# Optimization experiments

Hardware: AMD Instinct MI355X
Metric: run time of the kernel (lower is better)

The kernel has to match this reference:

```python
import jax, jax.numpy as jnp
import numpy as np

N, E, NF, EF, G = 50000, 400000, 128, 64, 200


def _leaky(x):
    return jax.nn.leaky_relu(x, 0.01)


def _edge_softmax(logits, dst, n):
    # softmax over edges grouped by destination node; logits: [E, 1]
    m = jax.ops.segment_max(logits, dst, num_segments=n)
    m = jnp.where(jnp.isfinite(m), m, 0.0)  # guard empty segments
    e = jnp.exp(logits - m[dst])
    s = jax.ops.segment_sum(e, dst, num_segments=n)
    return e / s[dst]


def _gru(x, h, Wx, Wh, bx, bh):
    # torch.nn.GRUCell gate order: (r, z, n)
    gx = x @ Wx + bx
    gh = h @ Wh + bh
    H = h.shape[-1]
    r = jax.nn.sigmoid(gx[:, :H] + gh[:, :H])
    z = jax.nn.sigmoid(gx[:, H:2 * H] + gh[:, H:2 * H])
    nn_ = jnp.tanh(gx[:, 2 * H:] + r * gh[:, 2 * H:])
    return (1.0 - z) * nn_ + z * h


def setup_inputs() -> dict:
    key = jax.random.key(0)
    ks = jax.random.split(key, 20)
    f32 = jnp.float32
    w = lambda k, s: (jax.random.normal(k, s) * 0.05).astype(f32)
    z = lambda s: jnp.zeros(s, f32)
    return {
        "node_feats": jax.random.normal(ks[0], (N, NF), f32),
        "edge_feats": jax.random.normal(ks[1], (E, EF), f32),
        "gc_node_W": w(ks[4], (NF, G)), "gc_node_b": z((G,)),
        "gc_e1_W": w(ks[5], (NF + EF, G)), "gc_e1_b": z((G,)),
        "gc_e2_W": w(ks[6], (2 * G, 1)), "gc_e2_b": z((1,)),
        "gc_et_W": w(ks[7], (G, G)), "gc_et_b": z((G,)),
        "gc_gru_Wx": w(ks[8], (G, 3 * G)), "gc_gru_Wh": w(ks[9], (G, 3 * G)),
        "gc_gru_bx": z((3 * G,)), "gc_gru_bh": z((3 * G,)),
        "l1_e_W": w(ks[10], (2 * G, 1)), "l1_e_b": z((1,)),
        "l1_pn_W": w(ks[11], (G, G)), "l1_pn_b": z((G,)),
        "l1_gru_Wx": w(ks[12], (G, 3 * G)), "l1_gru_Wh": w(ks[13], (G, 3 * G)),
        "l1_gru_bx": z((3 * G,)), "l1_gru_bh": z((3 * G,)),
        "l1_bn_g": jnp.ones((G,), f32), "l1_bn_b": z((G,)),
        "src": jax.random.randint(ks[2], (E,), 0, N, jnp.int32),
        "dst": jax.random.randint(ks[3], (E,), 0, N, jnp.int32),
    }


def reference(node_feats, edge_feats,
              gc_node_W, gc_node_b, gc_e1_W, gc_e1_b, gc_e2_W, gc_e2_b,
              gc_et_W, gc_et_b, gc_gru_Wx, gc_gru_Wh, gc_gru_bx, gc_gru_bh,
              l1_e_W, l1_e_b, l1_pn_W, l1_pn_b, l1_gru_Wx, l1_gru_Wh,
              l1_gru_bx, l1_gru_bh, l1_bn_g, l1_bn_b, src, dst):
    n = node_feats.shape[0]
    # ---- GetContext ----
    hv_new = _leaky(node_feats @ gc_node_W + gc_node_b)                      # [N, G]
    he1 = _leaky(jnp.concatenate([node_feats[src], edge_feats], 1)
                 @ gc_e1_W + gc_e1_b)                                        # [E, G]
    logits = _leaky(jnp.concatenate([hv_new[dst], he1], 1)
                    @ gc_e2_W + gc_e2_b)                                     # [E, 1]
    a = _edge_softmax(logits, dst, n)
    e = a * (he1 @ gc_et_W + gc_et_b)
    c = jax.ops.segment_sum(e, dst, num_segments=n)                          # [N, G]
    h0 = jax.nn.relu(_gru(jax.nn.elu(c), hv_new,
                          gc_gru_Wx, gc_gru_Wh, gc_gru_bx, gc_gru_bh))
    # ---- GNNLayer ----
    logits2 = _leaky(jnp.concatenate([h0[dst], h0[src]], 1) @ l1_e_W + l1_e_b)
    a2 = _edge_softmax(logits2, dst, n) + 1.0
    hvp = h0 @ l1_pn_W + l1_pn_b
    c2 = jax.ops.segment_sum(hvp[src] * a2, dst, num_segments=n)
    h1 = jax.nn.relu(_gru(jax.nn.elu(c2), h0,
                          l1_gru_Wx, l1_gru_Wh, l1_gru_bx, l1_gru_bh))
    # BatchNorm1d (training-mode batch stats, eps=1e-5)
    mu = h1.mean(0)
    var = h1.var(0)
    h1 = l1_bn_g * (h1 - mu) / jnp.sqrt(var + 1e-5) + l1_bn_b
    return h0 + h1
```

## Files before the change

kernel.cpp:

```cpp
#include <hip/hip_runtime.h>
#include <math.h>

#define G 200
#define NF 128
#define EF 64

typedef __attribute__((ext_vector_type(8))) short bf16x8;
typedef __attribute__((ext_vector_type(4))) float f32x4;

__device__ __forceinline__ float leakyf(float x) { return x > 0.f ? x : 0.01f * x; }
__device__ __forceinline__ float eluf(float x)   { return x > 0.f ? x : (expf(x) - 1.f); }
__device__ __forceinline__ float sigm(float x)   { return 1.f / (1.f + expf(-x)); }

__device__ __forceinline__ unsigned short f2bf(float x) {
    union { float f; unsigned int u; } v; v.f = x;
    unsigned int r = v.u + 0x7FFF + ((v.u >> 16) & 1);
    return (unsigned short)(r >> 16);
}
__device__ __forceinline__ float bf2f(unsigned short u) {
    union { unsigned int i; float f; } v; v.i = ((unsigned int)u) << 16;
    return v.f;
}
__device__ __forceinline__ unsigned int pk2(float a, float b) {
    return (unsigned int)f2bf(a) | ((unsigned int)f2bf(b) << 16);
}

__global__ __launch_bounds__(256) void tprep_k(
    const float* __restrict__ W, unsigned short* __restrict__ Wt,
    int Kreal, int kpad, int Nstride, int Nreal)
{
    int total = 208 * kpad;
    for (int i = blockIdx.x * 256 + threadIdx.x; i < total; i += gridDim.x * 256) {
        int n = i / kpad, k = i % kpad;
        Wt[i] = (n < Nreal && k < Kreal) ? f2bf(W[(size_t)k * Nstride + n]) : 0;
    }
}

__global__ __launch_bounds__(256) void wgru3_k(
    const float* __restrict__ Wx, const float* __restrict__ Wh,
    unsigned short* __restrict__ Btrz, unsigned short* __restrict__ Btn)
{
    const int total = 512 * 416;
    for (int i = blockIdx.x * 256 + threadIdx.x; i < total; i += gridDim.x * 256) {
        int n = i / 416, k = i % 416;
        float v = 0.f;
        if (n < 416) {
            int gg = (n >= 208) ? 1 : 0;
            int c = n - gg * 208;
            if (c < 200) {
                if (k < 200)                  v = Wx[(size_t)k * 600 + gg * 200 + c];
                else if (k >= 208 && k < 408) v = Wh[(size_t)(k - 208) * 600 + gg * 200 + c];
            }
        }
        Btrz[i] = f2bf(v);

        float u = 0.f;
        int s = n >> 4, cc = n & 15;
        if (s < 26) {
            int c = (s >> 1) * 16 + cc;
            if (c < 200) {
                if (!(s & 1)) { if (k < 200) u = Wx[(size_t)k * 600 + 400 + c]; }
                else { if (k >= 208 && k < 408) u = Wh[(size_t)(k - 208) * 600 + 400 + c]; }
            }
        }
        Btn[i] = f2bf(u);
    }
}

__global__ __launch_bounds__(256) void gpack_k(
    const float* __restrict__ X, const float* __restrict__ H,
    unsigned short* __restrict__ Apk, int M, int Mpad)
{
    const long total = (long)Mpad * 52;
    for (long i = (long)blockIdx.x * 256 + threadIdx.x; i < total;
         i += (long)gridDim.x * 256) {
        int row = (int)(i / 52), ch = (int)(i % 52);
        uint4 u = make_uint4(0, 0, 0, 0);
        if (row < M) {
            if (ch < 25) {
                const float4* xp = (const float4*)(X + (size_t)row * 200 + ch * 8);
                float4 a = xp[0], b = xp[1];
                u.x = pk2(eluf(a.x), eluf(a.y)); u.y = pk2(eluf(a.z), eluf(a.w));
                u.z = pk2(eluf(b.x), eluf(b.y)); u.w = pk2(eluf(b.z), eluf(b.w));
            } else if (ch >= 26 && ch < 51) {
                const float4* hp = (const float4*)(H + (size_t)row * 200 + (ch - 26) * 8);
                float4 a = hp[0], b = hp[1];
                u.x = pk2(a.x, a.y); u.y = pk2(a.z, a.w);
                u.z = pk2(b.x, b.y); u.w = pk2(b.z, b.w);
            }
        }
        *(uint4*)&Apk[(size_t)row * 416 + ch * 8] = u;
    }
}

template <int EPI>
__global__ __launch_bounds__(256) void tgemm_k(
    const unsigned short* __restrict__ Apk,
    const unsigned short* __restrict__ Bt,
    const float* __restrict__ bx, const float* __restrict__ bh,
    unsigned short* __restrict__ RZ,
    float* __restrict__ OUT, int M)
{
    __shared__ __align__(16) unsigned short As[2][128 * 32];
    __shared__ __align__(16) unsigned short Bs[2][128 * 32];

    const int tid = threadIdx.x;
    const int w = tid >> 6, lane = tid & 63, l15 = lane & 15, lq = lane >> 4;
    const int wr = w >> 1, wc = w & 1;
    const int bm = blockIdx.x * 128, bn = blockIdx.y * 128;
    const int r0 = tid >> 2, sl = tid & 3;

    f32x4 acc[4][4];
#pragma unroll
    for (int a = 0; a < 4; ++a)
#pragma unroll
        for (int b = 0; b < 4; ++b) acc[a][b] = (f32x4){0.f, 0.f, 0.f, 0.f};

    {
        uint4 pa0 = *(const uint4*)&Apk[(size_t)(bm + r0) * 416 + sl * 8];
        uint4 pa1 = *(const uint4*)&Apk[(size_t)(bm + 64 + r0) * 416 + sl * 8];
        uint4 pb0 = *(const uint4*)&Bt[(size_t)(bn + r0) * 416 + sl * 8];
        uint4 pb1 = *(const uint4*)&Bt[(size_t)(bn + 64 + r0) * 416 + sl * 8];
        int w0 = sl ^ ((r0 >> 1) & 3), w1 = sl ^ (((r0 + 64) >> 1) & 3);
        *(uint4*)&As[0][r0 * 32 + w0 * 8] = pa0;
        *(uint4*)&As[0][(r0 + 64) * 32 + w1 * 8] = pa1;
        *(uint4*)&Bs[0][r0 * 32 + w0 * 8] = pb0;
        *(uint4*)&Bs[0][(r0 + 64) * 32 + w1 * 8] = pb1;
    }
    __syncthreads();

    int cur = 0;
    for (int c = 0; c < 13; ++c) {
        uint4 pa0, pa1, pb0, pb1;
        if (c < 12) {
            int kc = (c + 1) * 32;
            pa0 = *(const uint4*)&Apk[(size_t)(bm + r0) * 416 + kc + sl * 8];
            pa1 = *(const uint4*)&Apk[(size_t)(bm + 64 + r0) * 416 + kc + sl * 8];
            pb0 = *(const uint4*)&Bt[(size_t)(bn + r0) * 416 + kc + sl * 8];
            pb1 = *(const uint4*)&Bt[(size_t)(bn + 64 + r0) * 416 + kc + sl * 8];
        }
        bf16x8 af[4], bfr[4];
#pragma unroll
        for (int s = 0; s < 4; ++s) {
            int ra = wr * 64 + s * 16 + l15;
            af[s] = *(const bf16x8*)&As[cur][ra * 32 + (lq ^ ((ra >> 1) & 3)) * 8];
            int rb = wc * 64 + s * 16 + l15;
            bfr[s] = *(const bf16x8*)&Bs[cur][rb * 32 + (lq ^ ((rb >> 1) & 3)) * 8];
        }
#pragma unroll
        for (int sr = 0; sr < 4; ++sr)
#pragma unroll
            for (int sc = 0; sc < 4; ++sc)
                acc[sr][sc] = __builtin_amdgcn_mfma_f32_16x16x32_bf16(
                    af[sr], bfr[sc], acc[sr][sc], 0, 0, 0);

        if (c < 12) {
            int nb = cur ^ 1;
            int w0 = sl ^ ((r0 >> 1) & 3), w1 = sl ^ (((r0 + 64) >> 1) & 3);
            *(uint4*)&As[nb][r0 * 32 + w0 * 8] = pa0;
            *(uint4*)&As[nb][(r0 + 64) * 32 + w1 * 8] = pa1;
            *(uint4*)&Bs[nb][r0 * 32 + w0 * 8] = pb0;
            *(uint4*)&Bs[nb][(r0 + 64) * 32 + w1 * 8] = pb1;
        }
        __syncthreads();
        cur ^= 1;
    }

    if (EPI == 0) {
#pragma unroll
        for (int sr = 0; sr < 4; ++sr)
#pragma unroll
            for (int sc = 0; sc < 4; ++sc) {
                int col = bn + wc * 64 + sc * 16 + l15;
                if (col >= 416) continue;
                float bsum = (col < 208) ? (bx[col] + bh[col])
                                         : (bx[col - 8] + bh[col - 8]);
#pragma unroll
                for (int i = 0; i < 4; ++i) {
                    int row = bm + wr * 64 + sr * 16 + lq * 4 + i;
                    if (row < M)
                        RZ[(size_t)row * 416 + col] = f2bf(sigm(acc[sr][sc][i] + bsum));
                }
            }
    } else {
#pragma unroll
        for (int p = 0; p < 2; ++p) {
            int sglob = (bn >> 4) + wc * 4 + 2 * p;
            int cc = (sglob >> 1) * 16 + l15;
            if (cc >= 200) continue;
            float bxn = bx[400 + cc], bhn = bh[400 + cc];
#pragma unroll
            for (int sr = 0; sr < 4; ++sr)
#pragma unroll
                for (int i = 0; i < 4; ++i) {
                    int row = bm + wr * 64 + sr * 16 + lq * 4 + i;
                    if (row >= M) continue;
                    float rr = bf2f(RZ[(size_t)row * 416 + cc]);
                    float zz = bf2f(RZ[(size_t)row * 416 + 208 + cc]);
                    float hh = bf2f(Apk[(size_t)row * 416 + 208 + cc]);
                    float nn = tanhf(acc[sr][2 * p][i] + bxn +
                                     rr * (acc[sr][2 * p + 1][i] + bhn));
                    float o = (1.f - zz) * nn + zz * hh;
                    OUT[(size_t)row * 200 + cc] = fmaxf(o, 0.f);
                }
        }
    }
}

__global__ __launch_bounds__(256) void hist_k(
    const int* __restrict__ dst, int* __restrict__ cnt, int E)
{
    int i = blockIdx.x * 256 + threadIdx.x;
    if (i < E) atomicAdd(&cnt[dst[i]], 1);
}

__global__ __launch_bounds__(256) void scan_k(
    const int* __restrict__ cnt, int* __restrict__ offs,
    int* __restrict__ cursor, int Nn)
{
    __shared__ int wsum[4];
    const int tid = threadIdx.x;
    const int lane = tid & 63, wv = tid >> 6;
    int carry = 0;
    const int CH = 8;
    for (int base = 0; base < Nn; base += 256 * CH) {
        int v[CH]; int tsum = 0;
        int i0 = base + tid * CH;
#pragma unroll
        for (int j = 0; j < CH; ++j) {
            v[j] = (i0 + j < Nn) ? cnt[i0 + j] : 0;
            tsum += v[j];
        }
        int x = tsum;
        for (int off = 1; off < 64; off <<= 1) {
            int t = __shfl_up(x, off);
            if (lane >= off) x += t;
        }
        if (lane == 63) wsum[wv] = x;
        __syncthreads();
        int wbase = 0;
#pragma unroll
        for (int wq = 0; wq < 4; ++wq) wbase += (wq < wv) ? wsum[wq] : 0;
        int gtot = wsum[0] + wsum[1] + wsum[2] + wsum[3];
        int run = carry + wbase + (x - tsum);
#pragma unroll
        for (int j = 0; j < CH; ++j) {
            int idx = i0 + j;
            if (idx < Nn) { offs[idx] = run; cursor[idx] = run; }
            run += v[j];
        }
        carry += gtot;
        __syncthreads();
    }
    if (tid == 0) offs[Nn] = carry;
}

__global__ __launch_bounds__(256) void scatter_k(
    const int* __restrict__ src, const int* __restrict__ dst,
    int* __restrict__ cursor, int* __restrict__ eidC,
    int* __restrict__ srcC, int* __restrict__ dstC, int E)
{
    int i = blockIdx.x * 256 + threadIdx.x;
    if (i < E) {
        int d = dst[i];
        int pos = atomicAdd(&cursor[d], 1);
        eidC[pos] = i; srcC[pos] = src[i]; dstC[pos] = d;
    }
}

__global__ __launch_bounds__(256) void mgemm_k(
    const float* __restrict__ X, const unsigned short* __restrict__ Wt,
    const float* __restrict__ bias, float* __restrict__ OUT,
    int M, int Kreal, int kch, int astr, int leaky,
    const float* __restrict__ xdiv)
{
    __shared__ __align__(16) unsigned short A[64 * 232];
    const int tid = threadIdx.x;
    const int w = tid >> 6, lane = tid & 63, l15 = lane & 15, lq = lane >> 4;
    const int bm = blockIdx.x * 64;
    const int kpad = kch * 32;
    const int nch8 = Kreal >> 3;

    for (int i = tid; i < 64 * nch8; i += 256) {
        int r = i / nch8, ch = i % nch8;
        int grow = bm + r;
        uint4 u = make_uint4(0, 0, 0, 0);
        if (grow < M) {
            const float4* xp = (const float4*)(X + (size_t)grow * Kreal + ch * 8);
            float inv = 1.f;
            if (xdiv) { float dv = xdiv[grow]; inv = (dv > 0.f) ? 1.f / dv : 0.f; }
            float4 a = xp[0], b = xp[1];
            u.x = pk2(a.x * inv, a.y * inv); u.y = pk2(a.z * inv, a.w * inv);
            u.z = pk2(b.x * inv, b.y * inv); u.w = pk2(b.z * inv, b.w * inv);
        }
        *(uint4*)&A[r * astr + ch * 8] = u;
    }
    if (tid < 64) {
        for (int p = Kreal; p < kpad; p += 8)
            *(uint4*)&A[tid * astr + p] = make_uint4(0, 0, 0, 0);
    }
    __syncthreads();

    const int arow = (w * 16 + l15) * astr;
    f32x4 acc[13];
#pragma unroll
    for (int t = 0; t < 13; ++t) acc[t] = (f32x4){0.f, 0.f, 0.f, 0.f};

    for (int c = 0; c < kch; ++c) {
        bf16x8 a = *(const bf16x8*)&A[arow + c * 32 + lq * 8];
#pragma unroll
        for (int t = 0; t < 13; ++t) {
            bf16x8 b = *(const bf16x8*)&Wt[(size_t)(t * 16 + l15) * kpad + c * 32 + lq * 8];
            acc[t] = __builtin_amdgcn_mfma_f32_16x16x32_bf16(a, b, acc[t], 0, 0, 0);
        }
    }

    float rg[4];
#pragma unroll
    for (int i = 0; i < 4; ++i) {
        int grow = bm + w * 16 + lq * 4 + i;
        rg[i] = 1.f;
        if (xdiv && grow < M) rg[i] = (xdiv[grow] > 0.f) ? 1.f : 0.f;
    }

#pragma unroll
    for (int t = 0; t < 13; ++t) {
        int col = t * 16 + l15;
        if (col >= 200) continue;
        float bs = bias[col];
#pragma unroll
        for (int i = 0; i < 4; ++i) {
            int grow = bm + w * 16 + lq * 4 + i;
            if (grow >= M) continue;
            float v = acc[t][i] + bs * rg[i];
            OUT[(size_t)grow * 200 + col] = leaky ? leakyf(v) : v;
        }
    }
}

__global__ __launch_bounds__(256) void hd_k(
    const float* __restrict__ x, const float* __restrict__ W,
    float* __restrict__ hd, int Nn)
{
    int wid = blockIdx.x * 4 + (threadIdx.x >> 6);
    int lane = threadIdx.x & 63;
    if (wid >= Nn) return;
    float s = 0.f;
    for (int j = lane; j < G; j += 64) s += x[(size_t)wid * G + j] * W[j];
    for (int off = 32; off; off >>= 1) s += __shfl_down(s, off);
    if (lane == 0) hd[wid] = s;
}

__global__ __launch_bounds__(256) void edgefuse2_k(
    const float* __restrict__ node, const float* __restrict__ edgef,
    const int* __restrict__ srcC, const int* __restrict__ dstC,
    const int* __restrict__ eidC,
    const unsigned short* __restrict__ W1t, const float* __restrict__ b1,
    const float* __restrict__ e2W, const float* __restrict__ e2b,
    const float* __restrict__ hd,
    float* __restrict__ sden, float* __restrict__ hacc, int E)
{
    __shared__ __align__(16) unsigned short U[64 * 216];
    __shared__ __align__(16) unsigned short Wt[208 * 40];
    __shared__ float rowlg[64];
    __shared__ float pexp_s[64];
    __shared__ int   dst_s[64];

    const int tid  = threadIdx.x;
    const int w    = tid >> 6;
    const int lane = tid & 63;
    const int l15  = lane & 15;
    const int lq   = lane >> 4;
    const int eb   = blockIdx.x * 64;

    {
        const int r4 = tid >> 2, q = tid & 3;
        const int pos = eb + r4;
        if (pos < E) {
            const int se = srcC[pos];
            const int ei = eidC[pos];
            const float4* np = (const float4*)(node + (size_t)se * NF);
            const float4* ep = (const float4*)(edgef + (size_t)ei * EF);
            uint4* rowp = (uint4*)(U + r4 * 216);
#pragma unroll
            for (int i = 0; i < 4; ++i) {
                float4 a = np[q * 8 + 2 * i];
                float4 b = np[q * 8 + 2 * i + 1];
                uint4 u; u.x = pk2(a.x, a.y); u.y = pk2(a.z, a.w);
                u.z = pk2(b.x, b.y); u.w = pk2(b.z, b.w);
                rowp[q * 4 + i] = u;
            }
            uint4* edp = (uint4*)(U + r4 * 216 + 128);
#pragma unroll
            for (int i = 0; i < 2; ++i) {
                float4 a = ep[q * 4 + 2 * i];
                float4 b = ep[q * 4 + 2 * i + 1];
                uint4 u; u.x = pk2(a.x, a.y); u.y = pk2(a.z, a.w);
                u.z = pk2(b.x, b.y); u.w = pk2(b.z, b.w);
                edp[q * 2 + i] = u;
            }
        } else {
            uint4 z = make_uint4(0, 0, 0, 0);
            uint4* rowp = (uint4*)(U + r4 * 216);
#pragma unroll
            for (int i = 0; i < 4; ++i) rowp[q * 4 + i] = z;
            uint4* edp = (uint4*)(U + r4 * 216 + 128);
            edp[q * 2] = z; edp[q * 2 + 1] = z;
        }
        if (tid < 64) dst_s[tid] = (eb + tid < E) ? dstC[eb + tid] : -1;
    }
    __syncthreads();

    f32x4 acc[13];
#pragma unroll
    for (int t = 0; t < 13; ++t) acc[t] = (f32x4){0.f, 0.f, 0.f, 0.f};

    for (int c = 0; c < 6; ++c) {
        for (int q = tid; q < 832; q += 256) {
            int n = q >> 2, s = q & 3;
            *(uint4*)(Wt + n * 40 + s * 8) =
                *(const uint4*)(W1t + (size_t)n * 192 + c * 32 + s * 8);
        }
        __syncthreads();
        bf16x8 a = *(const bf16x8*)(U + (w * 16 + l15) * 216 + c * 32 + lq * 8);
#pragma unroll
        for (int t = 0; t < 13; ++t) {
            bf16x8 b = *(const bf16x8*)(Wt + (t * 16 + l15) * 40 + lq * 8);
            acc[t] = __builtin_amdgcn_mfma_f32_16x16x32_bf16(a, b, acc[t], 0, 0, 0);
        }
        __syncthreads();
    }

    float p[4] = {0.f, 0.f, 0.f, 0.f};
#pragma unroll
    for (int t = 0; t < 13; ++t) {
        const int col = t * 16 + l15;
#pragma unroll
        for (int r = 0; r < 4; ++r) {
            const int row = w * 16 + lq * 4 + r;
            float v = 0.f;
            if (col < 200) {
                v = leakyf(acc[t][r] + b1[col]);
                p[r] = fmaf(v, e2W[200 + col], p[r]);
            }
            U[row * 216 + col] = f2bf(v);
        }
    }
#pragma unroll
    for (int r = 0; r < 4; ++r) {
        p[r] += __shfl_xor(p[r], 1);
        p[r] += __shfl_xor(p[r], 2);
        p[r] += __shfl_xor(p[r], 4);
        p[r] += __shfl_xor(p[r], 8);
    }
    if (l15 == 0) {
#pragma unroll
        for (int r = 0; r < 4; ++r) rowlg[w * 16 + lq * 4 + r] = p[r];
    }
    __syncthreads();

    if (tid < 64) {
        float pe = 0.f;
        if (eb + tid < E) {
            float l = leakyf(rowlg[tid] + hd[dst_s[tid]] + e2b[0]);
            pe = expf(l);
            atomicAdd(&sden[dst_s[tid]], pe);
        }
        pexp_s[tid] = pe;
    }
    __syncthreads();

    if (tid < 200) {
        const int c = tid;
        float s = 0.f;
        int cur = dst_s[0];
        for (int r = 0; r < 64; ++r) {
            int d = dst_s[r];
            if (d < 0) break;
            if (d != cur) {
                atomicAdd(&hacc[(size_t)cur * 200 + c], s);
                s = 0.f; cur = d;
            }
            s = fmaf(pexp_s[r], bf2f(U[r * 216 + c]), s);
        }
        atomicAdd(&hacc[(size_t)cur * 200 + c], s);
    }
}

__global__ __launch_bounds__(256) void layer2b_k(
    const float* __restrict__ hvp,
    const float* __restrict__ hd2, const float* __restrict__ hs,
    const float* __restrict__ b,
    const int* __restrict__ offs, const int* __restrict__ srcC,
    float* __restrict__ c2, int Nn)
{
    const int wv = threadIdx.x >> 6;
    const int lane = threadIdx.x & 63;
    const int n = blockIdx.x * 4 + wv;
    if (n >= Nn) return;

    const int base = offs[n], end = offs[n + 1];
    const float hdn = hd2[n] + b[0];

    float ss = 0.f;
    for (int pos = base + lane; pos < end; pos += 64)
        ss += expf(leakyf(hdn + hs[srcC[pos]]));
    for (int off = 32; off; off >>= 1) ss += __shfl_xor(ss, off);
    float inv = (end > base) ? 1.f / ss : 0.f;

    float a0 = 0.f, a1 = 0.f, a2v = 0.f, a3 = 0.f;
    for (int pos = base; pos < end; ++pos) {
        int sidx = srcC[pos];
        float pe = expf(leakyf(hdn + hs[sidx]));
        float aw = pe * inv + 1.f;
        const float* vr = hvp + (size_t)sidx * 200;
        a0  += aw * vr[lane];
        a1  += aw * vr[64 + lane];
        a2v += aw * vr[128 + lane];
        if (lane < 8) a3 += aw * vr[192 + lane];
    }
    float* out = c2 + (size_t)n * 200;
    out[lane] = a0; out[64 + lane] = a1; out[128 + lane] = a2v;
    if (lane < 8) out[192 + lane] = a3;
}

__global__ __launch_bounds__(256) void bnstat2_k(
    const float* __restrict__ h1, float* __restrict__ stats, int Nn)
{
    const int c = threadIdx.x;
    if (c >= 200) return;
    float s = 0.f, s2 = 0.f;
    for (int r = blockIdx.x; r < Nn; r += gridDim.x) {
        float v = h1[(size_t)r * 200 + c];
        s += v; s2 += v * v;
    }
    atomicAdd(&stats[c], s);
    atomicAdd(&stats[G + c], s2);
}

__global__ __launch_bounds__(256) void final_k(
    float* __restrict__ out, const float* __restrict__ h1,
    const float* __restrict__ stats,
    const float* __restrict__ g, const float* __restrict__ bb, int Nn)
{
    long total = (long)Nn * G;
    for (long idx = (long)blockIdx.x * 256 + threadIdx.x; idx < total;
         idx += (long)gridDim.x * 256) {
        int c = (int)(idx % G);
        float mu  = stats[c] / Nn;
        float var = stats[G + c] / Nn - mu * mu;
        float xh  = (h1[idx] - mu) * rsqrtf(var + 1e-5f);
        out[idx] = out[idx] + g[c] * xh + bb[c];
    }
}

extern "C" void kernel_launch(void* const* d_in, const int* in_sizes, int n_in,
                              void* d_out, int out_size, void* d_ws, size_t ws_size,
                              hipStream_t stream)
{
    const float* node_feats = (const float*)d_in[0];
    const float* edge_feats = (const float*)d_in[1];
    const float* gc_node_W  = (const float*)d_in[2];
    const float* gc_node_b  = (const float*)d_in[3];
    const float* gc_e1_W    = (const float*)d_in[4];
    const float* gc_e1_b    = (const float*)d_in[5];
    const float* gc_e2_W    = (const float*)d_in[6];
    const float* gc_e2_b    = (const float*)d_in[7];
    const float* gc_et_W    = (const float*)d_in[8];
    const float* gc_et_b    = (const float*)d_in[9];
    const float* gc_gru_Wx  = (const float*)d_in[10];
    const float* gc_gru_Wh  = (const float*)d_in[11];
    const float* gc_gru_bx  = (const float*)d_in[12];
    const float* gc_gru_bh  = (const float*)d_in[13];
    const float* l1_e_W     = (const float*)d_in[14];
    const float* l1_e_b     = (const float*)d_in[15];
    const float* l1_pn_W    = (const float*)d_in[16];
    const float* l1_pn_b    = (const float*)d_in[17];
    const float* l1_gru_Wx  = (const float*)d_in[18];
    const float* l1_gru_Wh  = (const float*)d_in[19];
    const float* l1_gru_bx  = (const float*)d_in[20];
    const float* l1_gru_bh  = (const float*)d_in[21];
    const float* l1_bn_g    = (const float*)d_in[22];
    const float* l1_bn_b    = (const float*)d_in[23];
    const int*   src        = (const int*)d_in[24];
    const int*   dst        = (const int*)d_in[25];

    const int Nn = in_sizes[0] / NF;
    const int E  = in_sizes[24];
    const int Mpad = ((Nn + 127) / 128) * 128;

    float* ws = (float*)d_ws;
    size_t o = 0;
    float* hv    = ws + o; o += (size_t)Nn * G;
    float* cbuf  = ws + o; o += ((size_t)Mpad * 416 + 1) / 2;
    unsigned short* rzbuf = (unsigned short*)cbuf;
    float* sden  = ws + o; o += (size_t)Nn;
    float* hd    = ws + o; o += (size_t)Nn;
    float* hs    = ws + o; o += (size_t)Nn;
    float* stats = ws + o; o += 512;
    unsigned short* W1t_g  = (unsigned short*)(ws + o); o += (208 * 192) / 2;
    unsigned short* etWt_g = (unsigned short*)(ws + o); o += (208 * 224) / 2;
    unsigned short* ncWt_g = (unsigned short*)(ws + o); o += (208 * 128) / 2;
    unsigned short* pnWt_g = (unsigned short*)(ws + o); o += (208 * 224) / 2;
    unsigned short* Btrz1  = (unsigned short*)(ws + o); o += (512 * 416) / 2;
    unsigned short* Btn1   = (unsigned short*)(ws + o); o += (512 * 416) / 2;
    unsigned short* Btrz2  = (unsigned short*)(ws + o); o += (512 * 416) / 2;
    unsigned short* Btn2   = (unsigned short*)(ws + o); o += (512 * 416) / 2;
    int* cnt    = (int*)(ws + o); o += (size_t)Nn;
    int* offs   = (int*)(ws + o); o += (size_t)Nn + 1;
    int* cursor = (int*)(ws + o); o += (size_t)Nn;
    int* eidC   = (int*)(ws + o); o += (size_t)E;
    int* srcC   = (int*)(ws + o); o += (size_t)E;
    int* dstC   = (int*)(ws + o); o += (size_t)E;
    unsigned short* apack = (unsigned short*)(ws + o); o += ((size_t)Mpad * 416 + 1) / 2;

    float* h0  = (float*)d_out;
    float* hvp = hv;
    float* h1  = hv;

    const int gN64 = (Nn + 63) / 64;
    const int gE64 = (E + 63) / 64;
    const int gE256 = (E + 255) / 256;
    const int nWaves = (Nn + 3) / 4;
    const long totNG = (long)Nn * G;
    const dim3 gGEMM((Mpad / 128), 4);

    hipMemsetAsync(cnt, 0, (size_t)Nn * sizeof(int), stream);
    tprep_k<<<128, 256, 0, stream>>>(gc_e1_W,   W1t_g,  192, 192, 200, 200);
    tprep_k<<<128, 256, 0, stream>>>(gc_et_W,   etWt_g, 200, 224, 200, 200);
    tprep_k<<<128, 256, 0, stream>>>(gc_node_W, ncWt_g, 128, 128, 200, 200);
    tprep_k<<<128, 256, 0, stream>>>(l1_pn_W,   pnWt_g, 200, 224, 200, 200);
    wgru3_k<<<256, 256, 0, stream>>>(gc_gru_Wx, gc_gru_Wh, Btrz1, Btn1);
    wgru3_k<<<256, 256, 0, stream>>>(l1_gru_Wx, l1_gru_Wh, Btrz2, Btn2);
    hist_k<<<gE256, 256, 0, stream>>>(dst, cnt, E);
    scan_k<<<1, 256, 0, stream>>>(cnt, offs, cursor, Nn);
    scatter_k<<<gE256, 256, 0, stream>>>(src, dst, cursor, eidC, srcC, dstC, E);

    hipMemsetAsync(sden, 0, (size_t)Nn * sizeof(float), stream);
    hipMemsetAsync(cbuf, 0, (size_t)Nn * G * sizeof(float), stream);
    hipMemsetAsync(stats, 0, 512 * sizeof(float), stream);

    mgemm_k<<<gN64, 256, 0, stream>>>(node_feats, ncWt_g, gc_node_b, hv,
                                      Nn, 128, 4, 136, 1, nullptr);
    hd_k<<<nWaves, 256, 0, stream>>>(hv, gc_e2_W, hd, Nn);

    edgefuse2_k<<<gE64, 256, 0, stream>>>(
        node_feats, edge_feats, srcC, dstC, eidC,
        W1t_g, gc_e1_b, gc_e2_W, gc_e2_b, hd, sden, cbuf, E);

    mgemm_k<<<gN64, 256, 0, stream>>>(cbuf, etWt_g, gc_et_b, cbuf,
                                      Nn, 200, 7, 232, 0, sden);

    gpack_k<<<2048, 256, 0, stream>>>(cbuf, hv, apack, Nn, Mpad);
    tgemm_k<0><<<gGEMM, 256, 0, stream>>>(apack, Btrz1, gc_gru_bx, gc_gru_bh,
                                          rzbuf, nullptr, Nn);
    tgemm_k<1><<<gGEMM, 256, 0, stream>>>(apack, Btn1, gc_gru_bx, gc_gru_bh,
                                          rzbuf, h0, Nn);

    hd_k<<<nWaves, 256, 0, stream>>>(h0, l1_e_W, hd, Nn);
    hd_k<<<nWaves, 256, 0, stream>>>(h0, l1_e_W + 200, hs, Nn);

    mgemm_k<<<gN64, 256, 0, stream>>>(h0, pnWt_g, l1_pn_b, hvp,
                                      Nn, 200, 7, 232, 0, nullptr);

    layer2b_k<<<nWaves, 256, 0, stream>>>(hvp, hd, hs, l1_e_b,
                                          offs, srcC, cbuf, Nn);

    gpack_k<<<2048, 256, 0, stream>>>(cbuf, h0, apack, Nn, Mpad);
    tgemm_k<0><<<gGEMM, 256, 0, stream>>>(apack, Btrz2, l1_gru_bx, l1_gru_bh,
                                          rzbuf, nullptr, Nn);
    tgemm_k<1><<<gGEMM, 256, 0, stream>>>(apack, Btn2, l1_gru_bx, l1_gru_bh,
                                          rzbuf, h1, Nn);

    bnstat2_k<<<512, 256, 0, stream>>>(h1, stats, Nn);
    final_k<<<2048, 256, 0, stream>>>((float*)d_out, h1, stats,
                                      l1_bn_g, l1_bn_b, Nn);
}
```

Baseline: 1.020 ms.

## Aggregate edge messages from MFMA registers, merge hd kernels, use fp16 gates

The edge kernel no longer writes activated messages to shared memory for a 200-thread serial aggregation. Each lane instead scatters its 4 accumulator rows directly, merging consecutive rows that share a destination before issuing atomics. This trades a serial LDS loop for more global atomics. The two hd dot-product launches are fused into one kernel that reads h0 once. The GRU r/z buffer switches from bf16 to fp16 for precision, and the hidden state is read from the fp32 source rather than from the bf16 packed operand.

```diff
diff --git a/kernel.cpp b/kernel.cpp
--- a/kernel.cpp
+++ b/kernel.cpp
@@ -98,7 +98,8 @@
     const unsigned short* __restrict__ Apk,
     const unsigned short* __restrict__ Bt,
     const float* __restrict__ bx, const float* __restrict__ bh,
-    unsigned short* __restrict__ RZ,
+    _Float16* __restrict__ RZ,
+    const float* __restrict__ Hf,
     float* __restrict__ OUT, int M)
 {
     __shared__ __align__(16) unsigned short As[2][128 * 32];
@@ -179,7 +180,8 @@
                 for (int i = 0; i < 4; ++i) {
                     int row = bm + wr * 64 + sr * 16 + lq * 4 + i;
                     if (row < M)
-                        RZ[(size_t)row * 416 + col] = f2bf(sigm(acc[sr][sc][i] + bsum));
+                        RZ[(size_t)row * 416 + col] =
+                            (_Float16)sigm(acc[sr][sc][i] + bsum);
                 }
             }
     } else {
@@ -195,9 +197,9 @@
                 for (int i = 0; i < 4; ++i) {
                     int row = bm + wr * 64 + sr * 16 + lq * 4 + i;
                     if (row >= M) continue;
-                    float rr = bf2f(RZ[(size_t)row * 416 + cc]);
-                    float zz = bf2f(RZ[(size_t)row * 416 + 208 + cc]);
-                    float hh = bf2f(Apk[(size_t)row * 416 + 208 + cc]);
+                    float rr = (float)RZ[(size_t)row * 416 + cc];
+                    float zz = (float)RZ[(size_t)row * 416 + 208 + cc];
+                    float hh = Hf[(size_t)row * 200 + cc];
                     float nn = tanhf(acc[sr][2 * p][i] + bxn +
                                      rr * (acc[sr][2 * p + 1][i] + bhn));
                     float o = (1.f - zz) * nn + zz * hh;
@@ -351,7 +353,27 @@
     if (lane == 0) hd[wid] = s;
 }
 
-__global__ __launch_bounds__(256) void edgefuse2_k(
+__global__ __launch_bounds__(256) void hdpair_k(
+    const float* __restrict__ x, const float* __restrict__ W,
+    float* __restrict__ hd2, float* __restrict__ hs, int Nn)
+{
+    int wid = blockIdx.x * 4 + (threadIdx.x >> 6);
+    int lane = threadIdx.x & 63;
+    if (wid >= Nn) return;
+    float s1 = 0.f, s2 = 0.f;
+    for (int j = lane; j < G; j += 64) {
+        float v = x[(size_t)wid * G + j];
+        s1 = fmaf(v, W[j], s1);
+        s2 = fmaf(v, W[200 + j], s2);
+    }
+    for (int off = 32; off; off >>= 1) {
+        s1 += __shfl_down(s1, off);
+        s2 += __shfl_down(s2, off);
+    }
+    if (lane == 0) { hd2[wid] = s1; hs[wid] = s2; }
+}
+
+__global__ __launch_bounds__(256) void edgefuse4_k(
     const float* __restrict__ node, const float* __restrict__ edgef,
     const int* __restrict__ srcC, const int* __restrict__ dstC,
     const int* __restrict__ eidC,
@@ -437,13 +459,12 @@
         const int col = t * 16 + l15;
 #pragma unroll
         for (int r = 0; r < 4; ++r) {
-            const int row = w * 16 + lq * 4 + r;
             float v = 0.f;
             if (col < 200) {
                 v = leakyf(acc[t][r] + b1[col]);
                 p[r] = fmaf(v, e2W[200 + col], p[r]);
             }
-            U[row * 216 + col] = f2bf(v);
+            acc[t][r] = v;
         }
     }
 #pragma unroll
@@ -470,20 +491,34 @@
     }
     __syncthreads();
 
-    if (tid < 200) {
-        const int c = tid;
-        float s = 0.f;
-        int cur = dst_s[0];
-        for (int r = 0; r < 64; ++r) {
-            int d = dst_s[r];
-            if (d < 0) break;
-            if (d != cur) {
-                atomicAdd(&hacc[(size_t)cur * 200 + c], s);
-                s = 0.f; cur = d;
-            }
-            s = fmaf(pexp_s[r], bf2f(U[r * 216 + c]), s);
-        }
-        atomicAdd(&hacc[(size_t)cur * 200 + c], s);
+    const int rbase = w * 16 + lq * 4;
+    const int d0 = dst_s[rbase + 0], d1 = dst_s[rbase + 1];
+    const int d2 = dst_s[rbase + 2], d3 = dst_s[rbase + 3];
+    const float pe0 = pexp_s[rbase + 0], pe1 = pexp_s[rbase + 1];
+    const float pe2 = pexp_s[rbase + 2], pe3 = pexp_s[rbase + 3];
+
+#pragma unroll
+    for (int t = 0; t < 13; ++t) {
+        const int col = t * 16 + l15;
+        if (col >= 200) continue;
+        float s = pe0 * acc[t][0];
+        int cur = d0;
+        if (d1 != cur) {
+            if (cur >= 0) atomicAdd(&hacc[(size_t)cur * 200 + col], s);
+            s = 0.f; cur = d1;
+        }
+        s = fmaf(pe1, acc[t][1], s);
+        if (d2 != cur) {
+            if (cur >= 0) atomicAdd(&hacc[(size_t)cur * 200 + col], s);
+            s = 0.f; cur = d2;
+        }
+        s = fmaf(pe2, acc[t][2], s);
+        if (d3 != cur) {
+            if (cur >= 0) atomicAdd(&hacc[(size_t)cur * 200 + col], s);
+            s = 0.f; cur = d3;
+        }
+        s = fmaf(pe3, acc[t][3], s);
+        if (cur >= 0) atomicAdd(&hacc[(size_t)cur * 200 + col], s);
     }
 }
 
@@ -593,7 +628,7 @@
     size_t o = 0;
     float* hv    = ws + o; o += (size_t)Nn * G;
     float* cbuf  = ws + o; o += ((size_t)Mpad * 416 + 1) / 2;
-    unsigned short* rzbuf = (unsigned short*)cbuf;
+    _Float16* rzbuf = (_Float16*)cbuf;
     float* sden  = ws + o; o += (size_t)Nn;
     float* hd    = ws + o; o += (size_t)Nn;
     float* hs    = ws + o; o += (size_t)Nn;
@@ -622,7 +657,6 @@
     const int gE64 = (E + 63) / 64;
     const int gE256 = (E + 255) / 256;
     const int nWaves = (Nn + 3) / 4;
-    const long totNG = (long)Nn * G;
     const dim3 gGEMM((Mpad / 128), 4);
 
     hipMemsetAsync(cnt, 0, (size_t)Nn * sizeof(int), stream);
@@ -644,7 +678,7 @@
                                       Nn, 128, 4, 136, 1, nullptr);
     hd_k<<<nWaves, 256, 0, stream>>>(hv, gc_e2_W, hd, Nn);
 
-    edgefuse2_k<<<gE64, 256, 0, stream>>>(
+    edgefuse4_k<<<gE64, 256, 0, stream>>>(
         node_feats, edge_feats, srcC, dstC, eidC,
         W1t_g, gc_e1_b, gc_e2_W, gc_e2_b, hd, sden, cbuf, E);
 
@@ -653,12 +687,11 @@
 
     gpack_k<<<2048, 256, 0, stream>>>(cbuf, hv, apack, Nn, Mpad);
     tgemm_k<0><<<gGEMM, 256, 0, stream>>>(apack, Btrz1, gc_gru_bx, gc_gru_bh,
-                                          rzbuf, nullptr, Nn);
+                                          rzbuf, nullptr, nullptr, Nn);
     tgemm_k<1><<<gGEMM, 256, 0, stream>>>(apack, Btn1, gc_gru_bx, gc_gru_bh,
-                                          rzbuf, h0, Nn);
-
-    hd_k<<<nWaves, 256, 0, stream>>>(h0, l1_e_W, hd, Nn);
-    hd_k<<<nWaves, 256, 0, stream>>>(h0, l1_e_W + 200, hs, Nn);
+                                          rzbuf, hv, h0, Nn);
+
+    hdpair_k<<<nWaves, 256, 0, stream>>>(h0, l1_e_W, hd, hs, Nn);
 
     mgemm_k<<<gN64, 256, 0, stream>>>(h0, pnWt_g, l1_pn_b, hvp,
                                       Nn, 200, 7, 232, 0, nullptr);
@@ -668,9 +701,9 @@
 
     gpack_k<<<2048, 256, 0, stream>>>(cbuf, h0, apack, Nn, Mpad);
     tgemm_k<0><<<gGEMM, 256, 0, stream>>>(apack, Btrz2, l1_gru_bx, l1_gru_bh,
-                                          rzbuf, nullptr, Nn);
+                                          rzbuf, nullptr, nullptr, Nn);
     tgemm_k<1><<<gGEMM, 256, 0, stream>>>(apack, Btn2, l1_gru_bx, l1_gru_bh,
-                                          rzbuf, h1, Nn);
+                                          rzbuf, h0, h1, Nn);
 
     bnstat2_k<<<512, 256, 0, stream>>>(h1, stats, Nn);
     final_k<<<2048, 256, 0, stream>>>((float*)d_out, h1, stats,
```

Result: slower. 1.104 ms (+8.2%).
